# Performance work log

Measured on AMD Instinct MI355X. Metric: run time of the kernel, lower is better.

Reference implementation:

```python
import jax, jax.numpy as jnp
import numpy as np

B, H, HKV, N, D = 1, 16, 4, 2048, 64
HID = H * D
CB = 16      # compress_block_size == selection_block_size
NSEL = 4     # num_selected_blocks
WIN = 64     # sliding_window_size
NEG = -1e10


def rmsnorm(x, scale):
    return x * jax.lax.rsqrt(jnp.mean(x * x, axis=-1, keepdims=True) + 1e-6) * scale


def setup_inputs() -> dict:
    key = jax.random.key(0)
    ks = jax.random.split(key, 8)
    return {
        "hidden": jax.random.normal(ks[0], (B, N, HID), jnp.float32),
        "q": jax.random.normal(ks[1], (B, H, N, D), jnp.float32),
        "k": jax.random.normal(ks[2], (B, HKV, N, D), jnp.float32),
        "v": jax.random.normal(ks[3], (B, HKV, N, D), jnp.float32),
        "compress_mem_kv": jax.random.normal(ks[4], (2, HKV, 1, D), jnp.float32) * 0.02,
        "k_norm_scale": jnp.ones((D,), jnp.float32),
        "v_norm_scale": jnp.ones((D,), jnp.float32),
        "combiner_w": jax.random.normal(ks[5], (3 * H, HID), jnp.float32) * 0.02,
        "combiner_b": jnp.tile(jnp.array([-5.0, -5.0, 5.0], jnp.float32), H),
        "combine_w": jax.random.normal(ks[6], (HID, HID), jnp.float32) * 0.02,
    }


def reference(hidden, q, k, v, compress_mem_kv, k_norm_scale, v_norm_scale, combiner_w, combiner_b, combine_w):
    b, h, n, d = q.shape
    hkv = k.shape[1]
    g = h // hkv
    scale = d ** -0.5
    w = n // CB  # number of compress / selection blocks
    qpos = jnp.arange(n)

    # --- mean-pool compression + RMSNorm (MeanPoolCompress) ---
    k_blocks = k[:, :, : w * CB].reshape(b, hkv, w, CB, d)
    v_blocks = v[:, :, : w * CB].reshape(b, hkv, w, CB, d)
    ck = rmsnorm(k_blocks.mean(3), k_norm_scale)  # [b,hkv,w,d]
    cv = rmsnorm(v_blocks.mean(3), v_norm_scale)

    # --- branch 1: compressed coarse attention (with 1 mem token) ---
    mem_k = jnp.broadcast_to(compress_mem_kv[0], (b, hkv, 1, d))
    mem_v = jnp.broadcast_to(compress_mem_kv[1], (b, hkv, 1, d))
    ck_full = jnp.repeat(jnp.concatenate([mem_k, ck], axis=2), g, axis=1)  # [b,h,1+w,d]
    cv_full = jnp.repeat(jnp.concatenate([mem_v, cv], axis=2), g, axis=1)
    sim_c = jnp.einsum('bhid,bhjd->bhij', q, ck_full) * scale
    block_end = jnp.arange(1, w + 1) * CB - 1
    causal = block_end[None, :] < qpos[:, None]  # [n,w]
    mask_c = jnp.concatenate([jnp.ones((n, 1), bool), causal], axis=1)
    sim_c = jnp.where(mask_c[None, None], sim_c, NEG)
    out_c = jnp.einsum('bhij,bhjd->bhid', jax.nn.softmax(sim_c, axis=-1), cv_full)
    importance = sim_c[..., 1:]  # [b,h,n,w] (mem token stripped)

    # --- branch 2: fine top-k block selection attention ---
    imp = importance.reshape(b, hkv, g, n, w).mean(2)  # GQA mean -> [b,hkv,n,w]
    imp = jax.nn.softmax(jnp.pad(imp, ((0, 0), (0, 0), (0, 0), (1, 0)), constant_values=NEG), axis=-1)[..., 1:]
    _, idx = jax.lax.top_k(imp, NSEL)  # [b,hkv,n,NSEL]
    bi = jnp.arange(b)[:, None, None, None]
    hi = jnp.arange(hkv)[None, :, None, None]
    sel_k = k_blocks[bi, hi, idx]  # [b,hkv,n,NSEL,CB,d] gather
    sel_v = v_blocks[bi, hi, idx]
    sel_k = jnp.repeat(sel_k, g, axis=1).reshape(b, h, n, NSEL * CB, d)
    sel_v = jnp.repeat(sel_v, g, axis=1).reshape(b, h, n, NSEL * CB, d)
    key_pos = idx[..., None] * CB + jnp.arange(CB)  # [b,hkv,n,NSEL,CB]
    key_pos = jnp.repeat(key_pos, g, axis=1).reshape(b, h, n, NSEL * CB)
    sim_f = jnp.einsum('bhid,bhikd->bhik', q, sel_k) * scale
    sim_f = jnp.where(key_pos <= qpos[None, None, :, None], sim_f, NEG)
    out_f = jnp.einsum('bhik,bhikd->bhid', jax.nn.softmax(sim_f, axis=-1), sel_v)

    # --- branch 3: causal sliding window attention ---
    k_full = jnp.repeat(k, g, axis=1)
    v_full = jnp.repeat(v, g, axis=1)
    sim_s = jnp.einsum('bhid,bhjd->bhij', q, k_full) * scale
    win_mask = (qpos[None, :] <= qpos[:, None]) & (qpos[None, :] > qpos[:, None] - WIN)
    sim_s = jnp.where(win_mask[None, None], sim_s, NEG)
    out_s = jnp.einsum('bhij,bhjd->bhid', jax.nn.softmax(sim_s, axis=-1), v_full)

    # --- sigmoid-gated branch combination + output projection ---
    gates = jax.nn.sigmoid(hidden @ combiner_w.T + combiner_b)  # [b,n,3h]
    gates = gates.reshape(b, n, h, 3).transpose(0, 2, 1, 3)     # [b,h,n,3]
    combined = gates[..., 0:1] * out_c + gates[..., 1:2] * out_f + gates[..., 2:3] * out_s
    out = combined.transpose(0, 2, 1, 3).reshape(b, n, h * d) @ combine_w.T
    return out
```

## Files before the change

kernel.cpp:

```cpp
#include <hip/hip_runtime.h>
#include <hip/hip_bf16.h>
#include <math.h>

#define H    16
#define HKV  4
#define G    4
#define NN   2048
#define D    64
#define HID  1024
#define CB   16
#define W    128
#define NSEL 4
#define WIN  64
#define NEGV -1e10f
#define SCALE 0.125f

typedef __attribute__((ext_vector_type(4))) float f32x4;
typedef __attribute__((ext_vector_type(4))) short short4v;
typedef __attribute__((ext_vector_type(8))) short short8v;

__device__ inline short f2b(float x){
    __hip_bfloat16 h = __float2bfloat16(x);
    return *reinterpret_cast<short*>(&h);
}
__device__ inline float b2f(short s){
    unsigned u = ((unsigned)(unsigned short)s) << 16;
    return __builtin_bit_cast(float, u);
}
__device__ inline short8v cvt8(f32x4 a, f32x4 b){
    short8v r;
    r[0]=f2b(a[0]); r[1]=f2b(a[1]); r[2]=f2b(a[2]); r[3]=f2b(a[3]);
    r[4]=f2b(b[0]); r[5]=f2b(b[1]); r[6]=f2b(b[2]); r[7]=f2b(b[3]);
    return r;
}
#define SWZ(byte, row) ((byte) ^ (((row)&7)<<4))
#define MFMA(a,b,c) __builtin_amdgcn_mfma_f32_16x16x32_bf16(a,b,c,0,0,0)

__device__ inline float wave_sum(float x){ for(int o=32;o;o>>=1) x += __shfl_xor(x,o); return x; }

__device__ inline f32x4 vmax4(f32x4 a, f32x4 b){
    f32x4 r; r[0]=fmaxf(a[0],b[0]); r[1]=fmaxf(a[1],b[1]); r[2]=fmaxf(a[2],b[2]); r[3]=fmaxf(a[3],b[3]); return r;
}
__device__ inline f32x4 shflx4(f32x4 x, int o){
    f32x4 r; r[0]=__shfl_xor(x[0],o); r[1]=__shfl_xor(x[1],o); r[2]=__shfl_xor(x[2],o); r[3]=__shfl_xor(x[3],o); return r;
}
__device__ inline f32x4 exp4(f32x4 x){
    f32x4 r; r[0]=expf(x[0]); r[1]=expf(x[1]); r[2]=expf(x[2]); r[3]=expf(x[3]); return r;
}

__device__ inline void conv_seg(const float* __restrict__ src, short* __restrict__ dst,
                                int b, int t){
    size_t idx = (size_t)b*1024 + t*4;
    f32x4 a = *(const f32x4*)(src + idx);
    short4v r; r[0]=f2b(a[0]); r[1]=f2b(a[1]); r[2]=f2b(a[2]); r[3]=f2b(a[3]);
    *(short4v*)(dst + idx) = r;
}

__global__ __launch_bounds__(256) void k_prep(
    const float* __restrict__ combiner_w,
    const float* __restrict__ k, const float* __restrict__ v,
    const float* __restrict__ memkv, const float* __restrict__ ksc, const float* __restrict__ vsc,
    short* __restrict__ cwb, short* __restrict__ kb16,
    short* __restrict__ vT, short* __restrict__ ckb, short* __restrict__ cvtg)
{
    int b = blockIdx.x, t = threadIdx.x;
    if (b < 48){ conv_seg(combiner_w, cwb, b, t); return; }
    b -= 48;
    if (b < 512){ conv_seg(k, kb16, b, t); return; }
    b -= 512;
    if (b < 128){
        __shared__ float tl[64][65];
        int hk = b>>5, i0 = (b&31)*64;
        for (int u=0;u<4;u++){
            int cid = t + 256*u; int r = cid>>4, ch = cid&15;
            f32x4 a = *(const f32x4*)(v + ((size_t)(hk*NN + i0 + r))*D + ch*4);
            tl[r][ch*4+0]=a[0]; tl[r][ch*4+1]=a[1]; tl[r][ch*4+2]=a[2]; tl[r][ch*4+3]=a[3];
        }
        __syncthreads();
        int d = t>>2, qd = t&3;
        short8v p0, p1;
        #pragma unroll
        for (int e=0;e<8;e++) p0[e] = f2b(tl[qd*16+e][d]);
        #pragma unroll
        for (int e=0;e<8;e++) p1[e] = f2b(tl[qd*16+8+e][d]);
        short* dst = vT + ((size_t)(hk*64 + d))*NN + i0 + qd*16;
        *(short8v*)dst = p0;
        *(short8v*)(dst+8) = p1;
        return;
    }
    b -= 128;
    {
        int j = b;
        int hk = t>>6, d = t&63;
        if (j > 128){
            if (j < 144) ckb[((size_t)(hk*144 + j))*64 + d] = 0;
            cvtg[((size_t)(hk*64 + d))*160 + j] = 0;
            return;
        }
        float xk, xv;
        if (j==0){ xk = memkv[(0*HKV+hk)*D + d]; xv = memkv[(HKV+hk)*D + d]; }
        else {
            int jb = j-1;
            const float* kp = k + ((size_t)(hk*NN + jb*CB))*D + d;
            const float* vp = v + ((size_t)(hk*NN + jb*CB))*D + d;
            float sk=0.f, sv=0.f;
            #pragma unroll
            for (int tt=0;tt<CB;tt++){ sk += kp[tt*D]; sv += vp[tt*D]; }
            xk = sk*(1.0f/CB); xv = sv*(1.0f/CB);
            float msk = wave_sum(xk*xk)*(1.0f/D);
            float msv = wave_sum(xv*xv)*(1.0f/D);
            xk = xk*rsqrtf(msk+1e-6f)*ksc[d];
            xv = xv*rsqrtf(msv+1e-6f)*vsc[d];
        }
        ckb[((size_t)(hk*144 + j))*64 + d] = f2b(xk);
        cvtg[((size_t)(hk*64 + d))*160 + j] = f2b(xv);
    }
}

__global__ __launch_bounds__(256, 4) void k_attn(
    const float* __restrict__ q, const short* __restrict__ ckb, const short* __restrict__ cvt_g,
    short* __restrict__ outc, int* __restrict__ selidx,
    const short* __restrict__ kb16, const short* __restrict__ vTg, short* __restrict__ outs,
    const float* __restrict__ hidden, const short* __restrict__ cwb,
    float* __restrict__ gpart,
    const float* __restrict__ combine_w, short* __restrict__ wbg)
{
    __shared__ char smem[35072];
    int b = blockIdx.x, t = threadIdx.x;
    int w = t>>6, lane = t&63, c = lane&15, lg = lane>>4;

    if (b >= 1152){ conv_seg(combine_w, wbg, b - 1152, t); return; }

    if (b < 512){
        char* aq  = smem;
        char* ckl = smem + 8192;
        char* pl  = smem;
        float* impl = (float*)(smem + 26624);
        float* psl  = (float*)(smem + 34816);
        int hk = b & 3, i0 = (b >> 2)*16;
        const short* cvhk = cvt_g + (size_t)hk*64*160;

        for (int u=0;u<2;u++){
            int cid = t + 256*u; int row = cid>>3, ch = cid&7;
            const float* src = q + ((size_t)((hk*G + (row&3))*NN + i0 + (row>>2)))*D + ch*8;
            f32x4 a = *(const f32x4*)src, bb2 = *(const f32x4*)(src+4);
            *(short8v*)(aq + SWZ(row*128 + ch*16, row)) = cvt8(a,bb2);
        }
        for (int u=0;u<5;u++){
            int cid = t + 256*u;
            if (cid < 1152){
                int row = cid>>3, ch = cid&7;
                const short* src = ckb + ((size_t)(hk*144 + row))*64 + ch*8;
                *(short8v*)(ckl + SWZ(row*128 + ch*16, row)) = *(const short8v*)src;
            }
        }
        __syncthreads();

        f32x4 acc[9];
        #pragma unroll
        for (int ct=0;ct<9;ct++) acc[ct] = (f32x4)0.f;
        #pragma unroll
        for (int ks=0;ks<2;ks++){
            int arow = w*16 + c;
            short8v af = *(short8v*)(aq + SWZ(arow*128 + ks*64 + lg*16, arow));
            #pragma unroll
            for (int ct=0;ct<9;ct++){
                int row = ct*16 + c;
                short8v bf = *(short8v*)(ckl + SWZ(row*128 + ks*64 + lg*16, row));
                acc[ct] = MFMA(af, bf, acc[ct]);
            }
        }

        f32x4 sum;
        {
            int tloc = w*4 + lg;
            int ii = i0 + tloc;
            #pragma unroll
            for (int ct=0;ct<9;ct++){
                int j = ct*16 + c;
                bool vis = (j==0) || (j<=128 && j*16 <= ii);
                f32x4 s = acc[ct]*SCALE;
                if (!vis){ s[0]=NEGV; s[1]=NEGV; s[2]=NEGV; s[3]=NEGV; }
                acc[ct] = s;
            }
            #pragma unroll
            for (int ct=0;ct<9;ct++){
                int j = ct*16 + c;
                if (j>=1 && j<=128){
                    f32x4 s = acc[ct];
                    impl[tloc*128 + (j-1)] = 0.25f*(s[0]+s[1]+s[2]+s[3]);
                }
            }
            f32x4 mx = acc[0];
            #pragma unroll
            for (int ct=1;ct<9;ct++) mx = vmax4(mx, acc[ct]);
            #pragma unroll
            for (int o=1;o<16;o<<=1) mx = vmax4(mx, shflx4(mx,o));
            sum = (f32x4)0.f;
            #pragma unroll
            for (int ct=0;ct<9;ct++){ acc[ct] = exp4(acc[ct]-mx); sum += acc[ct]; }
            #pragma unroll
            for (int o=1;o<16;o<<=1) sum += shflx4(sum,o);
        }
        __syncthreads();

        #pragma unroll
        for (int ct=0;ct<9;ct++){
            #pragma unroll
            for (int reg=0;reg<4;reg++){
                int row = w*16 + lg*4 + reg;
                *(short*)(pl + SWZ(row*320 + (ct*16+c)*2, row)) = f2b(acc[ct][reg]);
            }
        }
        #pragma unroll
        for (int reg=0;reg<4;reg++){
            int row = w*16 + lg*4 + reg;
            *(short*)(pl + SWZ(row*320 + (144+c)*2, row)) = 0;
        }
        if (c==0){
            #pragma unroll
            for (int reg=0;reg<4;reg++) psl[w*16 + lg*4 + reg] = sum[reg];
        }
        __syncthreads();

        {
            int tt = w*4 + lg;
            int sl = c;
            float vals[8];
            #pragma unroll
            for (int e=0;e<8;e++) vals[e] = impl[tt*128 + sl*8 + e];
            int sel[4];
            #pragma unroll
            for (int r4=0;r4<4;r4++){
                float bv = -INFINITY; int bj = 0;
                #pragma unroll
                for (int e=0;e<8;e++){
                    if (vals[e] > bv){ bv = vals[e]; bj = sl*8+e; }
                }
                #pragma unroll
                for (int o=1;o<16;o<<=1){
                    float ov = __shfl_xor(bv,o);
                    int oj = __shfl_xor(bj,o);
                    if (ov > bv || (ov==bv && oj<bj)){ bv=ov; bj=oj; }
                }
                sel[r4] = bj;
                if (sl == (bj>>3)){
                    #pragma unroll
                    for (int e=0;e<8;e++) if (e == (bj&7)) vals[e] = -INFINITY;
                }
            }
            if (sl == 0){
                int* sp = selidx + ((size_t)(hk*NN + i0 + tt))*NSEL;
                sp[0]=sel[0]; sp[1]=sel[1]; sp[2]=sel[2]; sp[3]=sel[3];
            }
        }

        f32x4 pv[4];
        #pragma unroll
        for (int ctd=0;ctd<4;ctd++) pv[ctd] = (f32x4)0.f;
        #pragma unroll
        for (int ks=0;ks<5;ks++){
            int arow = w*16 + c;
            short8v pf = *(short8v*)(pl + SWZ(arow*320 + ks*64 + lg*16, arow));
            #pragma unroll
            for (int ctd=0;ctd<4;ctd++){
                int row = ctd*16 + c;
                short8v bf = *(const short8v*)(cvhk + (size_t)row*160 + ks*32 + lg*8);
                pv[ctd] = MFMA(pf, bf, pv[ctd]);
            }
        }
        #pragma unroll
        for (int ctd=0;ctd<4;ctd++)
            #pragma unroll
            for (int reg=0;reg<4;reg++){
                int row = w*16 + lg*4 + reg;
                float inv = 1.0f/psl[row];
                int hh = hk*G + reg;
                int ii = i0 + (row>>2);
                outc[((size_t)(hh*NN + ii))*D + ctd*16 + c] = f2b(pv[ctd][reg]*inv);
            }
        return;
    }
    if (b < 1024){
        int idx = b - 512;
        char* aq = smem;
        char* kb = smem + 8192;
        float* psl = (float*)(smem + 24576);
        char* pl = kb;
        int i0 = (idx & 31)*64, h = idx >> 5;
        int hk = h >> 2;
        int pa = i0 - 64;
        for (int u=0;u<2;u++){
            int cid = t + 256*u; int row = cid>>3, ch = cid&7;
            const float* src = q + ((size_t)(h*NN + i0 + row))*D + ch*8;
            f32x4 a = *(const f32x4*)src, bb2 = *(const f32x4*)(src+4);
            *(short8v*)(aq + SWZ(row*128 + ch*16, row)) = cvt8(a,bb2);
        }
        for (int u=0;u<4;u++){
            int cid = t + 256*u; int row = cid>>3, ch = cid&7;
            int pos = pa + row; pos = pos < 0 ? 0 : pos;
            *(short8v*)(kb + SWZ(row*128 + ch*16, row)) =
                *(const short8v*)(kb16 + ((size_t)(hk*NN + pos))*D + ch*8);
        }
        __syncthreads();
        f32x4 acc[8];
        #pragma unroll
        for (int ct=0;ct<8;ct++) acc[ct] = (f32x4)0.f;
        #pragma unroll
        for (int ks=0;ks<2;ks++){
            int arow = w*16 + c;
            short8v af = *(short8v*)(aq + SWZ(arow*128 + ks*64 + lg*16, arow));
            #pragma unroll
            for (int ct=0;ct<8;ct++){
                int brow = ct*16 + c;
                short8v bf = *(short8v*)(kb + SWZ(brow*128 + ks*64 + lg*16, brow));
                acc[ct] = MFMA(af, bf, acc[ct]);
            }
        }
        #pragma unroll
        for (int ct=0;ct<8;ct++){
            int j = ct*16 + c;
            #pragma unroll
            for (int reg=0;reg<4;reg++){
                int tl2 = w*16 + lg*4 + reg;
                bool vis = (j >= tl2+1) && (j <= tl2+64) && (pa + j >= 0);
                float s = acc[ct][reg]*SCALE;
                acc[ct][reg] = vis ? s : NEGV;
            }
        }
        f32x4 mx = acc[0];
        #pragma unroll
        for (int ct=1;ct<8;ct++) mx = vmax4(mx, acc[ct]);
        #pragma unroll
        for (int o=1;o<16;o<<=1) mx = vmax4(mx, shflx4(mx,o));
        f32x4 sum = (f32x4)0.f;
        #pragma unroll
        for (int ct=0;ct<8;ct++){ acc[ct] = exp4(acc[ct]-mx); sum += acc[ct]; }
        #pragma unroll
        for (int o=1;o<16;o<<=1) sum += shflx4(sum,o);
        __syncthreads();
        #pragma unroll
        for (int ct=0;ct<8;ct++){
            #pragma unroll
            for (int reg=0;reg<4;reg++){
                int row = w*16 + lg*4 + reg;
                *(short*)(pl + SWZ(row*256 + (ct*16+c)*2, row)) = f2b(acc[ct][reg]);
            }
        }
        if (c==0){
            #pragma unroll
            for (int reg=0;reg<4;reg++) psl[w*16+lg*4+reg] = sum[reg];
        }
        __syncthreads();
        f32x4 pv[4];
        #pragma unroll
        for (int ctd=0;ctd<4;ctd++) pv[ctd] = (f32x4)0.f;
        #pragma unroll
        for (int ks=0;ks<4;ks++){
            int arow = w*16 + c;
            short8v pf = *(short8v*)(pl + SWZ(arow*256 + ks*64 + lg*16, arow));
            int pos0 = pa + ks*32 + lg*8;
            pos0 = pos0 < 0 ? 0 : pos0;
            #pragma unroll
            for (int ctd=0;ctd<4;ctd++){
                int d = ctd*16 + c;
                short8v bf = *(const short8v*)(vTg + ((size_t)(hk*64 + d))*NN + pos0);
                pv[ctd] = MFMA(pf, bf, pv[ctd]);
            }
        }
        #pragma unroll
        for (int ctd=0;ctd<4;ctd++)
            #pragma unroll
            for (int reg=0;reg<4;reg++){
                int row = w*16 + lg*4 + reg;
                float inv = 1.0f/psl[row];
                outs[((size_t)(h*NN + i0 + row))*D + ctd*16 + c] = f2b(pv[ctd][reg]*inv);
            }
        return;
    }
    {
        int idx = b - 1024;
        char* ha = smem;
        char* bl = smem + 8192;
        int i0g = (idx & 31)*64, ky = idx >> 5;
        f32x4 acc[3];
        #pragma unroll
        for (int ct=0;ct<3;ct++) acc[ct] = (f32x4)0.f;
        for (int kc=0;kc<4;kc++){
            int kbase = ky*256 + kc*64;
            if (kc) __syncthreads();
            for (int u=0;u<2;u++){
                int cid = t + 256*u; int row = cid>>3, ch = cid&7;
                const float* src = hidden + (size_t)(i0g+row)*HID + kbase + ch*8;
                f32x4 a = *(const f32x4*)src, bb2 = *(const f32x4*)(src+4);
                *(short8v*)(ha + SWZ(row*128 + ch*16, row)) = cvt8(a,bb2);
            }
            for (int u=0;u<2;u++){
                int cid = t + 256*u;
                if (cid < 384){
                    int row = cid>>3, ch = cid&7;
                    *(short8v*)(bl + SWZ(row*128 + ch*16, row)) =
                        *(const short8v*)(cwb + (size_t)row*HID + kbase + ch*8);
                }
            }
            __syncthreads();
            #pragma unroll
            for (int ks=0;ks<2;ks++){
                int arow = w*16 + c;
                short8v af = *(short8v*)(ha + SWZ(arow*128 + ks*64 + lg*16, arow));
                #pragma unroll
                for (int ct=0;ct<3;ct++){
                    int brow = ct*16 + c;
                    short8v bf = *(short8v*)(bl + SWZ(brow*128 + ks*64 + lg*16, brow));
                    acc[ct] = MFMA(af, bf, acc[ct]);
                }
            }
        }
        #pragma unroll
        for (int ct=0;ct<3;ct++)
            #pragma unroll
            for (int reg=0;reg<4;reg++){
                int row = w*16 + lg*4 + reg;
                gpart[((size_t)ky*NN + i0g + row)*48 + ct*16 + c] = acc[ct][reg];
            }
    }
}

__global__ __launch_bounds__(256) void k_selc(
    const float* __restrict__ q, const short* __restrict__ kbg, const short* __restrict__ vTg,
    const int* __restrict__ selidx,
    const short* __restrict__ outc, const short* __restrict__ outs,
    const float* __restrict__ gpart, const float* __restrict__ cbias,
    short* __restrict__ comb)
{
    __shared__ short pls[4][4*64];
    __shared__ float gsl[4][12];
    int i0 = blockIdx.x*4, hk = blockIdx.y, t = threadIdx.x;
    int wv = t>>6, lane = t&63;
    int i = i0 + wv;
    int c = lane&15, lg = lane>>4;
    int head = c & 3;

    int sel_r[4];
    #pragma unroll
    for (int nt=0;nt<4;nt++) sel_r[nt] = selidx[((size_t)(hk*NN + i))*NSEL + nt];

    short8v qa[2];
    #pragma unroll
    for (int ks=0;ks<2;ks++){
        const float* src = q + ((size_t)((hk*G + head)*NN + i))*D + ks*32 + lg*8;
        f32x4 a = *(const f32x4*)src, b = *(const f32x4*)(src+4);
        qa[ks] = cvt8(a,b);
    }

    f32x4 acc[4];
    #pragma unroll
    for (int nt=0;nt<4;nt++) acc[nt] = (f32x4)0.f;
    #pragma unroll
    for (int ks=0;ks<2;ks++){
        #pragma unroll
        for (int nt=0;nt<4;nt++){
            int pos = sel_r[nt]*CB + c;
            short8v bf = *(const short8v*)(kbg + ((size_t)(hk*NN + pos))*D + ks*32 + lg*8);
            acc[nt] = MFMA(qa[ks], bf, acc[nt]);
        }
    }
    #pragma unroll
    for (int nt=0;nt<4;nt++){
        int pos = sel_r[nt]*CB + c;
        f32x4 s = acc[nt]*SCALE;
        if (pos > i){ s[0]=NEGV; s[1]=NEGV; s[2]=NEGV; s[3]=NEGV; }
        acc[nt] = s;
    }
    f32x4 mx = acc[0];
    #pragma unroll
    for (int nt=1;nt<4;nt++) mx = vmax4(mx, acc[nt]);
    #pragma unroll
    for (int o=1;o<16;o<<=1) mx = vmax4(mx, shflx4(mx,o));
    f32x4 sum = (f32x4)0.f;
    #pragma unroll
    for (int nt=0;nt<4;nt++){ acc[nt] = exp4(acc[nt]-mx); sum += acc[nt]; }
    #pragma unroll
    for (int o=1;o<16;o<<=1) sum += shflx4(sum,o);

    if (lane < 16){
        #pragma unroll
        for (int nt=0;nt<4;nt++)
            #pragma unroll
            for (int reg=0;reg<4;reg++)
                pls[wv][reg*64 + nt*16 + lane] = f2b(acc[nt][reg]);
    }
    if (lane < 12){
        int o = hk*12 + lane;
        const float* gp0 = gpart + (size_t)i*48;
        float s = gp0[o] + gp0[(size_t)1*NN*48 + o]
                + gp0[(size_t)2*NN*48 + o] + gp0[(size_t)3*NN*48 + o] + cbias[o];
        gsl[wv][lane] = 1.0f/(1.0f+expf(-s));
    }
    __syncthreads();

    f32x4 pv[4];
    #pragma unroll
    for (int nt=0;nt<4;nt++) pv[nt] = (f32x4)0.f;
    #pragma unroll
    for (int ks=0;ks<2;ks++){
        short8v pa = *(const short8v*)(&pls[wv][head*64 + ks*32 + lg*8]);
        int sb = ks*2 + (lg>>1);
        int pos0 = sel_r[sb]*CB + (lg&1)*8;
        #pragma unroll
        for (int nt=0;nt<4;nt++){
            int d = nt*16 + c;
            short8v bf = *(const short8v*)(vTg + ((size_t)(hk*64 + d))*NN + pos0);
            pv[nt] = MFMA(pa, bf, pv[nt]);
        }
    }

    f32x4 myv = (lg==0) ? pv[0] : (lg==1) ? pv[1] : (lg==2) ? pv[2] : pv[3];
    int d = lg*16 + c;
    #pragma unroll
    for (int reg=0;reg<4;reg++){
        float g0 = gsl[wv][reg*3+0], g1 = gsl[wv][reg*3+1], g2 = gsl[wv][reg*3+2];
        size_t off = ((size_t)((hk*G+reg)*NN + i))*D + d;
        float fo = myv[reg] * (1.0f/sum[reg]);
        float val = g0*b2f(outc[off]) + g1*fo + g2*b2f(outs[off]);
        comb[(size_t)i*HID + (hk*G+reg)*64 + d] = f2b(val);
    }
}

__global__ __launch_bounds__(256) void k_gemm(
    const short* __restrict__ A, const short* __restrict__ Bw, float* __restrict__ out)
{
    __shared__ char ab[2][64*128];
    __shared__ char bb[2][64*128];
    int m0 = blockIdx.x*64, n0 = blockIdx.y*64, t = threadIdx.x;
    int w = t>>6, lane = t&63, c = lane&15, lg = lane>>4;
    int r0 = t>>3, ch0 = t&7;
    f32x4 acc[4];
    #pragma unroll
    for (int ct=0;ct<4;ct++) acc[ct] = (f32x4)0.f;
    const short* Ap = A  + (size_t)(m0+r0)*HID + ch0*8;
    const short* Bp = Bw + (size_t)(n0+r0)*HID + ch0*8;
    short8v ra0 = *(const short8v*)(Ap);
    short8v ra1 = *(const short8v*)(Ap + 32*HID);
    short8v rb0 = *(const short8v*)(Bp);
    short8v rb1 = *(const short8v*)(Bp + 32*HID);
    for (int kc=0;kc<16;kc++){
        char* abuf = ab[kc&1];
        char* bbuf = bb[kc&1];
        *(short8v*)(abuf + SWZ(r0*128 + ch0*16, r0)) = ra0;
        *(short8v*)(abuf + SWZ((r0+32)*128 + ch0*16, r0+32)) = ra1;
        *(short8v*)(bbuf + SWZ(r0*128 + ch0*16, r0)) = rb0;
        *(short8v*)(bbuf + SWZ((r0+32)*128 + ch0*16, r0+32)) = rb1;
        __syncthreads();
        if (kc < 15){
            const short* Ap2 = Ap + (kc+1)*64;
            const short* Bp2 = Bp + (kc+1)*64;
            ra0 = *(const short8v*)(Ap2);
            ra1 = *(const short8v*)(Ap2 + 32*HID);
            rb0 = *(const short8v*)(Bp2);
            rb1 = *(const short8v*)(Bp2 + 32*HID);
        }
        #pragma unroll
        for (int ks=0;ks<2;ks++){
            int arow = w*16 + c;
            short8v af = *(short8v*)(abuf + SWZ(arow*128 + ks*64 + lg*16, arow));
            #pragma unroll
            for (int ct=0;ct<4;ct++){
                int brow = ct*16 + c;
                short8v bf = *(short8v*)(bbuf + SWZ(brow*128 + ks*64 + lg*16, brow));
                acc[ct] = MFMA(af, bf, acc[ct]);
            }
        }
    }
    #pragma unroll
    for (int ct=0;ct<4;ct++)
        #pragma unroll
        for (int reg=0;reg<4;reg++){
            int row = w*16 + lg*4 + reg;
            out[((size_t)(m0+row))*HID + n0 + ct*16 + c] = acc[ct][reg];
        }
}

extern "C" void kernel_launch(void* const* d_in, const int* in_sizes, int n_in,
                              void* d_out, int out_size, void* d_ws, size_t ws_size,
                              hipStream_t stream)
{
    const float* hidden     = (const float*)d_in[0];
    const float* q          = (const float*)d_in[1];
    const float* k          = (const float*)d_in[2];
    const float* v          = (const float*)d_in[3];
    const float* memkv      = (const float*)d_in[4];
    const float* ksc        = (const float*)d_in[5];
    const float* vsc        = (const float*)d_in[6];
    const float* combiner_w = (const float*)d_in[7];
    const float* combiner_b = (const float*)d_in[8];
    const float* combine_w  = (const float*)d_in[9];
    float* out = (float*)d_out;

    char* p = (char*)d_ws;
    short* ckb  = (short*)p; p += (size_t)HKV*144*64*2;
    short* cvtg = (short*)p; p += (size_t)HKV*64*160*2;
    short* wbg  = (short*)p; p += (size_t)HID*HID*2;
    short* cwbg = (short*)p; p += (size_t)48*HID*2;
    short* kbg  = (short*)p; p += (size_t)HKV*NN*D*2;
    short* vTg  = (short*)p; p += (size_t)HKV*64*NN*2;
    short* outc = (short*)p; p += (size_t)H*NN*D*2;
    short* outs = (short*)p; p += (size_t)H*NN*D*2;
    float* gpart= (float*)p; p += (size_t)4*NN*48*4;
    short* comb = (short*)p; p += (size_t)NN*HID*2;
    int*  selix = (int*)p;   p += (size_t)HKV*NN*NSEL*4;

    k_prep <<<848, 256, 0, stream>>>(combiner_w, k, v, memkv, ksc, vsc,
                                      cwbg, kbg, vTg, ckb, cvtg);
    k_attn <<<2176, 256, 0, stream>>>(q, ckb, cvtg, outc, selix,
                                       kbg, vTg, outs, hidden, cwbg, gpart,
                                       combine_w, wbg);
    k_selc <<<dim3(NN/4, HKV), 256, 0, stream>>>(q, kbg, vTg, selix, outc, outs,
                                                  gpart, combiner_b, comb);
    k_gemm <<<dim3(NN/64, HID/64), 256, 0, stream>>>(comb, wbg, out);
}
```

Measured before the change: 65.96 us.

## Read MFMA B-operands directly from global memory instead of staging in LDS

In the compressed-attention, sliding-window and gate-GEMM segments of k_attn, the K/compressed-K/combiner-weight B fragments are now loaded straight from global (bf16) into registers rather than first copied into shared memory. The probability buffer is moved to a separate LDS region so two __syncthreads barriers per segment can be dropped. This removes LDS staging traffic and barriers, at the cost of redundant global/L2 reads across waves and possibly less coalesced access.

```diff
diff --git a/kernel.cpp b/kernel.cpp
--- a/kernel.cpp
+++ b/kernel.cpp
@@ -125,7 +125,7 @@
     float* __restrict__ gpart,
     const float* __restrict__ combine_w, short* __restrict__ wbg)
 {
-    __shared__ char smem[35072];
+    __shared__ char smem[37120];
     int b = blockIdx.x, t = threadIdx.x;
     int w = t>>6, lane = t&63, c = lane&15, lg = lane>>4;
 
@@ -133,11 +133,11 @@
 
     if (b < 512){
         char* aq  = smem;
-        char* ckl = smem + 8192;
-        char* pl  = smem;
-        float* impl = (float*)(smem + 26624);
-        float* psl  = (float*)(smem + 34816);
+        char* pl  = smem + 8192;
+        float* impl = (float*)(smem + 28672);
+        float* psl  = (float*)(smem + 36864);
         int hk = b & 3, i0 = (b >> 2)*16;
+        const short* ckhk = ckb + (size_t)hk*144*64;
         const short* cvhk = cvt_g + (size_t)hk*64*160;
 
         for (int u=0;u<2;u++){
@@ -146,14 +146,6 @@
             f32x4 a = *(const f32x4*)src, bb2 = *(const f32x4*)(src+4);
             *(short8v*)(aq + SWZ(row*128 + ch*16, row)) = cvt8(a,bb2);
         }
-        for (int u=0;u<5;u++){
-            int cid = t + 256*u;
-            if (cid < 1152){
-                int row = cid>>3, ch = cid&7;
-                const short* src = ckb + ((size_t)(hk*144 + row))*64 + ch*8;
-                *(short8v*)(ckl + SWZ(row*128 + ch*16, row)) = *(const short8v*)src;
-            }
-        }
         __syncthreads();
 
         f32x4 acc[9];
@@ -166,7 +158,7 @@
             #pragma unroll
             for (int ct=0;ct<9;ct++){
                 int row = ct*16 + c;
-                short8v bf = *(short8v*)(ckl + SWZ(row*128 + ks*64 + lg*16, row));
+                short8v bf = *(const short8v*)(ckhk + (size_t)row*64 + ks*32 + lg*8);
                 acc[ct] = MFMA(af, bf, acc[ct]);
             }
         }
@@ -202,7 +194,6 @@
             #pragma unroll
             for (int o=1;o<16;o<<=1) sum += shflx4(sum,o);
         }
-        __syncthreads();
 
         #pragma unroll
         for (int ct=0;ct<9;ct++){
@@ -221,7 +212,6 @@
             #pragma unroll
             for (int reg=0;reg<4;reg++) psl[w*16 + lg*4 + reg] = sum[reg];
         }
-        __syncthreads();
 
         {
             int tt = w*4 + lg;
@@ -284,25 +274,20 @@
     if (b < 1024){
         int idx = b - 512;
         char* aq = smem;
-        char* kb = smem + 8192;
+        char* pl = smem + 8192;
         float* psl = (float*)(smem + 24576);
-        char* pl = kb;
         int i0 = (idx & 31)*64, h = idx >> 5;
         int hk = h >> 2;
         int pa = i0 - 64;
+        const short* khk = kb16 + (size_t)hk*NN*64;
         for (int u=0;u<2;u++){
             int cid = t + 256*u; int row = cid>>3, ch = cid&7;
             const float* src = q + ((size_t)(h*NN + i0 + row))*D + ch*8;
             f32x4 a = *(const f32x4*)src, bb2 = *(const f32x4*)(src+4);
             *(short8v*)(aq + SWZ(row*128 + ch*16, row)) = cvt8(a,bb2);
         }
-        for (int u=0;u<4;u++){
-            int cid = t + 256*u; int row = cid>>3, ch = cid&7;
-            int pos = pa + row; pos = pos < 0 ? 0 : pos;
-            *(short8v*)(kb + SWZ(row*128 + ch*16, row)) =
-                *(const short8v*)(kb16 + ((size_t)(hk*NN + pos))*D + ch*8);
-        }
         __syncthreads();
+
         f32x4 acc[8];
         #pragma unroll
         for (int ct=0;ct<8;ct++) acc[ct] = (f32x4)0.f;
@@ -312,8 +297,9 @@
             short8v af = *(short8v*)(aq + SWZ(arow*128 + ks*64 + lg*16, arow));
             #pragma unroll
             for (int ct=0;ct<8;ct++){
-                int brow = ct*16 + c;
-                short8v bf = *(short8v*)(kb + SWZ(brow*128 + ks*64 + lg*16, brow));
+                int j = ct*16 + c;
+                int pos = pa + j; pos = pos < 0 ? 0 : pos;
+                short8v bf = *(const short8v*)(khk + (size_t)pos*64 + ks*32 + lg*8);
                 acc[ct] = MFMA(af, bf, acc[ct]);
             }
         }
@@ -338,7 +324,7 @@
         for (int ct=0;ct<8;ct++){ acc[ct] = exp4(acc[ct]-mx); sum += acc[ct]; }
         #pragma unroll
         for (int o=1;o<16;o<<=1) sum += shflx4(sum,o);
-        __syncthreads();
+
         #pragma unroll
         for (int ct=0;ct<8;ct++){
             #pragma unroll
@@ -351,7 +337,7 @@
             #pragma unroll
             for (int reg=0;reg<4;reg++) psl[w*16+lg*4+reg] = sum[reg];
         }
-        __syncthreads();
+
         f32x4 pv[4];
         #pragma unroll
         for (int ctd=0;ctd<4;ctd++) pv[ctd] = (f32x4)0.f;
@@ -381,7 +367,6 @@
     {
         int idx = b - 1024;
         char* ha = smem;
-        char* bl = smem + 8192;
         int i0g = (idx & 31)*64, ky = idx >> 5;
         f32x4 acc[3];
         #pragma unroll
@@ -395,14 +380,6 @@
                 f32x4 a = *(const f32x4*)src, bb2 = *(const f32x4*)(src+4);
                 *(short8v*)(ha + SWZ(row*128 + ch*16, row)) = cvt8(a,bb2);
             }
-            for (int u=0;u<2;u++){
-                int cid = t + 256*u;
-                if (cid < 384){
-                    int row = cid>>3, ch = cid&7;
-                    *(short8v*)(bl + SWZ(row*128 + ch*16, row)) =
-                        *(const short8v*)(cwb + (size_t)row*HID + kbase + ch*8);
-                }
-            }
             __syncthreads();
             #pragma unroll
             for (int ks=0;ks<2;ks++){
@@ -411,7 +388,7 @@
                 #pragma unroll
                 for (int ct=0;ct<3;ct++){
                     int brow = ct*16 + c;
-                    short8v bf = *(short8v*)(bl + SWZ(brow*128 + ks*64 + lg*16, brow));
+                    short8v bf = *(const short8v*)(cwb + (size_t)brow*HID + kbase + ks*32 + lg*8);
                     acc[ct] = MFMA(af, bf, acc[ct]);
                 }
             }
```

Result: slower. 69.86 us (+5.9%).
